# Kernel tuning notes

Hardware: AMD Instinct MI355X
Metric: run time of the kernel (lower is better)

Reference implementation:

```python
import jax, jax.numpy as jnp
import numpy as np
from jax import lax


def _conv(x, w, b):
    # x: [N,C,H,W], w: [O,I,kh,kw], valid conv, stride 1
    y = lax.conv_general_dilated(x, w, (1, 1), 'VALID',
                                 dimension_numbers=('NCHW', 'OIHW', 'NCHW'))
    return y + b[None, :, None, None]


def _maxpool2(x):
    return lax.reduce_window(x, -jnp.inf, lax.max, (1, 1, 2, 2), (1, 1, 2, 2), 'VALID')


def _affine_grid(theta, H, W):
    # torch F.affine_grid, align_corners=False: pixel-center normalized coords
    dt = theta.dtype
    xs = (2.0 * jnp.arange(W, dtype=dt) + 1.0) / W - 1.0  # [W]
    ys = (2.0 * jnp.arange(H, dtype=dt) + 1.0) / H - 1.0  # [H]
    gx = (theta[:, 0, 0][:, None, None] * xs[None, None, :]
          + theta[:, 0, 1][:, None, None] * ys[None, :, None]
          + theta[:, 0, 2][:, None, None])  # [N,H,W]
    gy = (theta[:, 1, 0][:, None, None] * xs[None, None, :]
          + theta[:, 1, 1][:, None, None] * ys[None, :, None]
          + theta[:, 1, 2][:, None, None])  # [N,H,W]
    return gx, gy


def _grid_sample(img, gx, gy):
    # torch F.grid_sample, bilinear, zeros padding, align_corners=False
    N, C, H, W = img.shape
    ix = ((gx + 1.0) * W - 1.0) * 0.5
    iy = ((gy + 1.0) * H - 1.0) * 0.5
    x0 = jnp.floor(ix)
    y0 = jnp.floor(iy)
    x1 = x0 + 1.0
    y1 = y0 + 1.0
    wx1 = ix - x0
    wx0 = 1.0 - wx1
    wy1 = iy - y0
    wy0 = 1.0 - wy1
    flat = img.reshape(N, C, H * W)

    def tap(xf, yf):
        xi = xf.astype(jnp.int32)
        yi = yf.astype(jnp.int32)
        inb = (xi >= 0) & (xi < W) & (yi >= 0) & (yi < H)
        idx = jnp.clip(yi, 0, H - 1) * W + jnp.clip(xi, 0, W - 1)  # [N,H,W]
        v = jnp.take_along_axis(flat, idx.reshape(N, 1, H * W), axis=2)
        return v.reshape(N, C, H, W) * inb.astype(img.dtype)[:, None]

    out = (tap(x0, y0) * (wx0 * wy0)[:, None]
           + tap(x1, y0) * (wx1 * wy0)[:, None]
           + tap(x0, y1) * (wx0 * wy1)[:, None]
           + tap(x1, y1) * (wx1 * wy1)[:, None])
    return out


def setup_inputs() -> dict:
    key = jax.random.key(0)
    ks = jax.random.split(key, 8)
    b, n, d, c = 64, 256, 28, 3
    x = jax.random.normal(ks[0], (b, n, d, d, c), dtype=jnp.float32)
    conv1_w = jax.random.normal(ks[1], (8, 3, 7, 7), dtype=jnp.float32) * 0.08
    conv1_b = jnp.zeros((8,), dtype=jnp.float32)
    conv2_w = jax.random.normal(ks[2], (10, 8, 5, 5), dtype=jnp.float32) * 0.07
    conv2_b = jnp.zeros((10,), dtype=jnp.float32)
    fc1_w = jax.random.normal(ks[3], (32, 90), dtype=jnp.float32) * 0.1
    fc1_b = jnp.zeros((32,), dtype=jnp.float32)
    # fc2 initialized near identity transform (as in the torch module),
    # with a small perturbation so theta depends on the input
    fc2_w = jax.random.normal(ks[4], (6, 32), dtype=jnp.float32) * 0.01
    fc2_b = jnp.array([1.0, 0.0, 0.0, 0.0, 1.0, 0.0], dtype=jnp.float32)
    return {"x": x, "conv1_w": conv1_w, "conv1_b": conv1_b,
            "conv2_w": conv2_w, "conv2_b": conv2_b,
            "fc1_w": fc1_w, "fc1_b": fc1_b,
            "fc2_w": fc2_w, "fc2_b": fc2_b}


def reference(x, conv1_w, conv1_b, conv2_w, conv2_b, fc1_w, fc1_b, fc2_w, fc2_b):
    b, n, d, _, c = x.shape
    xi = x.reshape(-1, d, d, c).transpose(0, 3, 1, 2)  # [b*n, 3, 28, 28]
    # localization net: conv -> maxpool -> relu, twice
    h = jax.nn.relu(_maxpool2(_conv(xi, conv1_w, conv1_b)))   # [N,8,11,11]
    h = jax.nn.relu(_maxpool2(_conv(h, conv2_w, conv2_b)))    # [N,10,3,3]
    h = h.reshape(-1, 10 * 3 * 3)
    h = jax.nn.relu(h @ fc1_w.T + fc1_b)
    theta = (h @ fc2_w.T + fc2_b).reshape(-1, 2, 3)
    gx, gy = _affine_grid(theta, d, d)
    out = _grid_sample(xi, gx, gy)                            # [N,3,28,28]
    return out.transpose(0, 2, 3, 1).reshape(b, n, d, d, c)
```

## Files before the change

### kernel.cpp

```cpp
#include <hip/hip_runtime.h>


typedef _Float16 half2_t __attribute__((ext_vector_type(2)));

static __device__ inline half2_t h2(uint32_t u) {
    union { uint32_t u; half2_t h; } cv; cv.u = u; return cv.h;
}

#if __has_builtin(__builtin_amdgcn_fdot2)
#define FDOT2(a, b, c) __builtin_amdgcn_fdot2((a), (b), (c), false)
#else
#define FDOT2(a, b, c) ((float)(a)[0] * (float)(b)[0] + (float)(a)[1] * (float)(b)[1] + (c))
#endif

__launch_bounds__(256, 4)
__global__ void stn_loc_kernel(
    const float* __restrict__ x,
    const float* __restrict__ w1, const float* __restrict__ b1,
    const float* __restrict__ w2, const float* __restrict__ b2,
    const float* __restrict__ fc1w, const float* __restrict__ fc1b,
    const float* __restrict__ fc2w, const float* __restrict__ fc2b,
    float* __restrict__ theta_ws)
{
    __shared__ __align__(16) _Float16 s_imgh[3 * 28 * 40];
    __shared__ __align__(16) uint32_t s_w1p[8 * 21 * 4];
    __shared__ __align__(16) float s_h1[8 * 11 * 12];
    __shared__ float s_h2[90];
    __shared__ float s_fch[32];

    const int t = threadIdx.x;
    const int n = blockIdx.x;
    const float* img = x + (size_t)n * 2352;

    for (int idx = t; idx < 504; idx += 256) {
        const int cc = idx / 168;
        const int rem = idx - 168 * cc;
        const int hh = rem / 6;
        const int kk = rem - 6 * hh;
        ((uint32_t*)s_imgh)[(((cc * 28 + hh) * 40) + 28 + 2 * kk) >> 1] = 0u;
    }
    for (int p = t; p < 784; p += 256) {
        const int h = p / 28, w = p - 28 * h;
        const float v0 = img[3 * p + 0];
        const float v1 = img[3 * p + 1];
        const float v2 = img[3 * p + 2];
        s_imgh[(0 * 28 + h) * 40 + w] = (_Float16)v0;
        s_imgh[(1 * 28 + h) * 40 + w] = (_Float16)v1;
        s_imgh[(2 * 28 + h) * 40 + w] = (_Float16)v2;
    }
    for (int idx = t; idx < 672; idx += 256) {
        const int o = idx / 84;  const int rem = idx - 84 * o;
        const int c = rem / 28;  const int r2 = rem - 28 * c;
        const int kh = r2 >> 2;  const int p = r2 & 3;
        const int k0 = 2 * p;
        const float* wbase = &w1[((o * 3 + c) * 7 + kh) * 7];
        const float wa = wbase[k0];
        const float wb = (k0 + 1 < 7) ? wbase[k0 + 1] : 0.0f;
        union { half2_t h; uint32_t u; } cv;
        cv.h = (half2_t){(_Float16)wa, (_Float16)wb};
        s_w1p[idx] = cv.u;
    }
    __syncthreads();

    if (t < 176) {
        const int i = t >> 3, o = t & 7;
        float acc[22];
        const float bias = b1[o];
        #pragma unroll
        for (int j = 0; j < 22; ++j) acc[j] = bias;

        for (int c = 0; c < 3; ++c) {
            #pragma unroll
            for (int kh = 0; kh < 7; ++kh) {
                const uint32_t* rowu =
                    (const uint32_t*)&s_imgh[(c * 28 + i + kh) * 40];
                uint32_t E[16];
                {
                    const uint4 a = ((const uint4*)rowu)[0];
                    const uint4 b = ((const uint4*)rowu)[1];
                    const uint4 cq = ((const uint4*)rowu)[2];
                    const uint4 d = ((const uint4*)rowu)[3];
                    E[0] = a.x;  E[1] = a.y;  E[2] = a.z;  E[3] = a.w;
                    E[4] = b.x;  E[5] = b.y;  E[6] = b.z;  E[7] = b.w;
                    E[8] = cq.x; E[9] = cq.y; E[10] = cq.z; E[11] = cq.w;
                    E[12] = d.x; E[13] = d.y; E[14] = d.z; E[15] = d.w;
                }
                uint32_t O[14];
                #pragma unroll
                for (int k = 0; k < 14; ++k)
                    O[k] = (E[k] >> 16) | (E[k + 1] << 16);

                const uint4 wq = *(const uint4*)&s_w1p[(o * 21 + c * 7 + kh) * 4];
                const half2_t wp0 = h2(wq.x), wp1 = h2(wq.y);
                const half2_t wp2 = h2(wq.z), wp3 = h2(wq.w);

                #pragma unroll
                for (int j = 0; j < 22; j += 2) {
                    const int b0 = j >> 1;
                    acc[j]     = FDOT2(h2(E[b0]),     wp0, acc[j]);
                    acc[j]     = FDOT2(h2(E[b0 + 1]), wp1, acc[j]);
                    acc[j]     = FDOT2(h2(E[b0 + 2]), wp2, acc[j]);
                    acc[j]     = FDOT2(h2(E[b0 + 3]), wp3, acc[j]);
                    acc[j + 1] = FDOT2(h2(O[b0]),     wp0, acc[j + 1]);
                    acc[j + 1] = FDOT2(h2(O[b0 + 1]), wp1, acc[j + 1]);
                    acc[j + 1] = FDOT2(h2(O[b0 + 2]), wp2, acc[j + 1]);
                    acc[j + 1] = FDOT2(h2(O[b0 + 3]), wp3, acc[j + 1]);
                }
            }
        }
        float hm[11];
        #pragma unroll
        for (int j = 0; j < 11; ++j) hm[j] = fmaxf(acc[2 * j], acc[2 * j + 1]);
        #pragma unroll
        for (int j = 0; j < 11; ++j) {
            float v = __shfl_xor(hm[j], 8);
            hm[j] = fmaxf(hm[j], v);
        }
        if ((i & 1) == 0) {
            float* row = &s_h1[(o * 11 + (i >> 1)) * 12];
            #pragma unroll
            for (int j = 0; j < 11; ++j) row[j] = fmaxf(hm[j], 0.0f);
        }
    }
    __syncthreads();

    if (t < 60) {
        const int o = t / 6, i = t - 6 * (t / 6);
        float acc2[6];
        const float bias = b2[o];
        #pragma unroll
        for (int j = 0; j < 6; ++j) acc2[j] = bias;
        for (int c = 0; c < 8; ++c) {
            #pragma unroll
            for (int kh = 0; kh < 5; ++kh) {
                const float* hrow = &s_h1[(c * 11 + i + kh) * 12];
                float im2[12];
                #pragma unroll
                for (int qq = 0; qq < 3; ++qq) {
                    float4 v = ((const float4*)hrow)[qq];
                    im2[4 * qq + 0] = v.x; im2[4 * qq + 1] = v.y;
                    im2[4 * qq + 2] = v.z; im2[4 * qq + 3] = v.w;
                }
                const float* wr = &w2[(o * 8 + c) * 25 + kh * 5];
                float wv[5];
                #pragma unroll
                for (int qq = 0; qq < 5; ++qq) wv[qq] = wr[qq];
                #pragma unroll
                for (int kw = 0; kw < 5; ++kw) {
                    #pragma unroll
                    for (int j = 0; j < 6; ++j)
                        acc2[j] += im2[j + kw] * wv[kw];
                }
            }
        }
        float hp[3];
        #pragma unroll
        for (int qq = 0; qq < 3; ++qq) hp[qq] = fmaxf(acc2[2 * qq], acc2[2 * qq + 1]);
        #pragma unroll
        for (int qq = 0; qq < 3; ++qq) {
            float v = __shfl_xor(hp[qq], 1);
            hp[qq] = fmaxf(hp[qq], v);
        }
        if ((i & 1) == 0) {
            #pragma unroll
            for (int qq = 0; qq < 3; ++qq)
                s_h2[o * 9 + (i >> 1) * 3 + qq] = fmaxf(hp[qq], 0.0f);
        }
    }
    __syncthreads();

    {
        const int of = t >> 3, l = t & 7;
        float acc = 0.0f;
        const float* wr = &fc1w[of * 90];
        #pragma unroll
        for (int m = 0; m < 12; ++m) {
            int j = l + 8 * m;
            if (j < 90) acc += s_h2[j] * wr[j];
        }
        acc += __shfl_xor(acc, 1);
        acc += __shfl_xor(acc, 2);
        acc += __shfl_xor(acc, 4);
        if (l == 0) s_fch[of] = fmaxf(acc + fc1b[of], 0.0f);
    }
    __syncthreads();

    if (t < 48) {
        const int of = t >> 3, l = t & 7;
        float acc = 0.0f;
        const float* wr = &fc2w[of * 32];
        #pragma unroll
        for (int m = 0; m < 4; ++m) {
            int j = l + 8 * m;
            acc += s_fch[j] * wr[j];
        }
        acc += __shfl_xor(acc, 1);
        acc += __shfl_xor(acc, 2);
        acc += __shfl_xor(acc, 4);
        if (l == 0) theta_ws[(size_t)n * 6 + of] = acc + fc2b[of];
    }
}

__launch_bounds__(256)
__global__ void stn_sample_kernel(
    const float* __restrict__ x,
    const float* __restrict__ theta_ws,
    float* __restrict__ out)
{
    const int t = threadIdx.x;
    const int n = blockIdx.x;
    const float* tw = theta_ws + (size_t)n * 6;
    const float t00 = tw[0], t01 = tw[1], t02 = tw[2];
    const float t10 = tw[3], t11 = tw[4], t12 = tw[5];
    const float* img = x + (size_t)n * 2352;
    float* outp = out + (size_t)n * 2352;

    for (int p = t; p < 784; p += 256) {
        int h = p / 28, w = p - 28 * h;
        float xs = (2.0f * w + 1.0f) * (1.0f / 28.0f) - 1.0f;
        float ys = (2.0f * h + 1.0f) * (1.0f / 28.0f) - 1.0f;
        float gx = t00 * xs + t01 * ys + t02;
        float gy = t10 * xs + t11 * ys + t12;
        float ix = ((gx + 1.0f) * 28.0f - 1.0f) * 0.5f;
        float iy = ((gy + 1.0f) * 28.0f - 1.0f) * 0.5f;
        float x0f = floorf(ix), y0f = floorf(iy);
        float wx1 = ix - x0f, wx0 = 1.0f - wx1;
        float wy1 = iy - y0f, wy0 = 1.0f - wy1;
        int x0 = (int)x0f, y0 = (int)y0f;
        int x1 = x0 + 1, y1 = y0 + 1;
        float fx0 = (x0 >= 0 && x0 < 28) ? 1.0f : 0.0f;
        float fx1 = (x1 >= 0 && x1 < 28) ? 1.0f : 0.0f;
        float fy0 = (y0 >= 0 && y0 < 28) ? 1.0f : 0.0f;
        float fy1 = (y1 >= 0 && y1 < 28) ? 1.0f : 0.0f;
        float w00 = wx0 * wy0 * fx0 * fy0;
        float w10 = wx1 * wy0 * fx1 * fy0;
        float w01 = wx0 * wy1 * fx0 * fy1;
        float w11 = wx1 * wy1 * fx1 * fy1;
        int cx0 = min(max(x0, 0), 27), cx1 = min(max(x1, 0), 27);
        int cy0 = min(max(y0, 0), 27), cy1 = min(max(y1, 0), 27);
        const float* p00 = img + (cy0 * 28 + cx0) * 3;
        const float* p10 = img + (cy0 * 28 + cx1) * 3;
        const float* p01 = img + (cy1 * 28 + cx0) * 3;
        const float* p11 = img + (cy1 * 28 + cx1) * 3;
        float* o3 = outp + 3 * p;
        #pragma unroll
        for (int c = 0; c < 3; ++c) {
            o3[c] = p00[c] * w00 + p10[c] * w10 + p01[c] * w01 + p11[c] * w11;
        }
    }
}

extern "C" void kernel_launch(void* const* d_in, const int* in_sizes, int n_in,
                              void* d_out, int out_size, void* d_ws, size_t ws_size,
                              hipStream_t stream) {
    const float* x     = (const float*)d_in[0];
    const float* w1    = (const float*)d_in[1];
    const float* b1    = (const float*)d_in[2];
    const float* w2    = (const float*)d_in[3];
    const float* b2    = (const float*)d_in[4];
    const float* fc1w  = (const float*)d_in[5];
    const float* fc1b  = (const float*)d_in[6];
    const float* fc2w  = (const float*)d_in[7];
    const float* fc2b  = (const float*)d_in[8];
    float* outp  = (float*)d_out;
    float* theta = (float*)d_ws;

    const int n_img = 64 * 256;
    stn_loc_kernel<<<dim3(n_img), dim3(256), 0, stream>>>(
        x, w1, b1, w2, b2, fc1w, fc1b, fc2w, fc2b, theta);
    stn_sample_kernel<<<dim3(n_img), dim3(256), 0, stream>>>(x, theta, outp);
}
```

Before: 313.2 us.

## Pack conv2 and fc1 operands as fp16 pairs and use fdot2

```diff
diff --git a/kernel.cpp b/kernel.cpp
--- a/kernel.cpp
+++ b/kernel.cpp
@@ -5,6 +5,11 @@
 
 static __device__ inline half2_t h2(uint32_t u) {
     union { uint32_t u; half2_t h; } cv; cv.u = u; return cv.h;
+}
+static __device__ inline uint32_t packh2(float a, float b) {
+    union { half2_t h; uint32_t u; } cv;
+    cv.h = (half2_t){(_Float16)a, (_Float16)b};
+    return cv.u;
 }
 
 #if __has_builtin(__builtin_amdgcn_fdot2)
@@ -24,8 +29,10 @@
 {
     __shared__ __align__(16) _Float16 s_imgh[3 * 28 * 40];
     __shared__ __align__(16) uint32_t s_w1p[8 * 21 * 4];
-    __shared__ __align__(16) float s_h1[8 * 11 * 12];
-    __shared__ float s_h2[90];
+    __shared__ __align__(16) uint32_t s_h1p[4 * 11 * 12];
+    __shared__ __align__(16) uint32_t s_w2p[4 * 5 * 10 * 8];
+    __shared__ __align__(16) uint32_t s_fc1wp[32 * 49];
+    __shared__ __align__(16) uint32_t s_h2p[64];
     __shared__ float s_fch[32];
 
     const int t = threadIdx.x;
@@ -56,18 +63,38 @@
         const float* wbase = &w1[((o * 3 + c) * 7 + kh) * 7];
         const float wa = wbase[k0];
         const float wb = (k0 + 1 < 7) ? wbase[k0 + 1] : 0.0f;
-        union { half2_t h; uint32_t u; } cv;
-        cv.h = (half2_t){(_Float16)wa, (_Float16)wb};
-        s_w1p[idx] = cv.u;
-    }
+        s_w1p[idx] = packh2(wa, wb);
+    }
+    for (int k = t; k < 1600; k += 256) {
+        const int kw = k & 7;
+        const int r = k >> 3;
+        const int o = r % 10;
+        const int ck = r / 10;
+        const int kh = ck % 5;
+        const int c2 = ck / 5;
+        uint32_t v = 0;
+        if (kw < 5) {
+            const float wa = w2[((o * 8 + 2 * c2) * 5 + kh) * 5 + kw];
+            const float wb = w2[((o * 8 + 2 * c2 + 1) * 5 + kh) * 5 + kw];
+            v = packh2(wa, wb);
+        }
+        s_w2p[k] = v;
+    }
+    for (int k = t; k < 1568; k += 256) {
+        const int of = k / 49;
+        const int j = k - 49 * of;
+        uint32_t v = 0;
+        if (j < 45) v = packh2(fc1w[of * 90 + 2 * j], fc1w[of * 90 + 2 * j + 1]);
+        s_fc1wp[k] = v;
+    }
+    if (t < 64) s_h2p[t] = 0;
     __syncthreads();
 
     if (t < 176) {
         const int i = t >> 3, o = t & 7;
         float acc[22];
-        const float bias = b1[o];
-        #pragma unroll
-        for (int j = 0; j < 22; ++j) acc[j] = bias;
+        #pragma unroll
+        for (int j = 0; j < 22; ++j) acc[j] = 0.0f;
 
         for (int c = 0; c < 3; ++c) {
             #pragma unroll
@@ -108,6 +135,7 @@
                 }
             }
         }
+        const float bias = b1[o];
         float hm[11];
         #pragma unroll
         for (int j = 0; j < 11; ++j) hm[j] = fmaxf(acc[2 * j], acc[2 * j + 1]);
@@ -117,9 +145,11 @@
             hm[j] = fmaxf(hm[j], v);
         }
         if ((i & 1) == 0) {
-            float* row = &s_h1[(o * 11 + (i >> 1)) * 12];
+            const int c2 = o >> 1, hf = o & 1, u = i >> 1;
+            _Float16* dst = ((_Float16*)s_h1p) + ((c2 * 11 + u) * 12) * 2 + hf;
             #pragma unroll
-            for (int j = 0; j < 11; ++j) row[j] = fmaxf(hm[j], 0.0f);
+            for (int m = 0; m < 11; ++m)
+                dst[2 * m] = (_Float16)fmaxf(hm[m] + bias, 0.0f);
         }
     }
     __syncthreads();
@@ -127,44 +157,53 @@
     if (t < 60) {
         const int o = t / 6, i = t - 6 * (t / 6);
         float acc2[6];
-        const float bias = b2[o];
-        #pragma unroll
-        for (int j = 0; j < 6; ++j) acc2[j] = bias;
-        for (int c = 0; c < 8; ++c) {
+        #pragma unroll
+        for (int j = 0; j < 6; ++j) acc2[j] = 0.0f;
+        #pragma unroll
+        for (int c2 = 0; c2 < 4; ++c2) {
             #pragma unroll
             for (int kh = 0; kh < 5; ++kh) {
-                const float* hrow = &s_h1[(c * 11 + i + kh) * 12];
-                float im2[12];
+                const uint32_t* row = &s_h1p[(c2 * 11 + i + kh) * 12];
+                uint32_t E[12];
+                {
+                    const uint4 a = ((const uint4*)row)[0];
+                    const uint4 b = ((const uint4*)row)[1];
+                    const uint4 cq = ((const uint4*)row)[2];
+                    E[0] = a.x;  E[1] = a.y;  E[2] = a.z;  E[3] = a.w;
+                    E[4] = b.x;  E[5] = b.y;  E[6] = b.z;  E[7] = b.w;
+                    E[8] = cq.x; E[9] = cq.y; E[10] = cq.z; E[11] = cq.w;
+                }
+                const uint32_t* wb = &s_w2p[((c2 * 5 + kh) * 10 + o) * 8];
+                const uint4 wq = *(const uint4*)wb;
+                const uint32_t w4 = wb[4];
+                const half2_t wp0 = h2(wq.x), wp1 = h2(wq.y), wp2 = h2(wq.z),
+                              wp3 = h2(wq.w), wp4 = h2(w4);
                 #pragma unroll
-                for (int qq = 0; qq < 3; ++qq) {
-                    float4 v = ((const float4*)hrow)[qq];
-                    im2[4 * qq + 0] = v.x; im2[4 * qq + 1] = v.y;
-                    im2[4 * qq + 2] = v.z; im2[4 * qq + 3] = v.w;
-                }
-                const float* wr = &w2[(o * 8 + c) * 25 + kh * 5];
-                float wv[5];
-                #pragma unroll
-                for (int qq = 0; qq < 5; ++qq) wv[qq] = wr[qq];
-                #pragma unroll
-                for (int kw = 0; kw < 5; ++kw) {
-                    #pragma unroll
-                    for (int j = 0; j < 6; ++j)
-                        acc2[j] += im2[j + kw] * wv[kw];
+                for (int j = 0; j < 6; ++j) {
+                    float a = acc2[j];
+                    a = FDOT2(h2(E[j]),     wp0, a);
+                    a = FDOT2(h2(E[j + 1]), wp1, a);
+                    a = FDOT2(h2(E[j + 2]), wp2, a);
+                    a = FDOT2(h2(E[j + 3]), wp3, a);
+                    a = FDOT2(h2(E[j + 4]), wp4, a);
+                    acc2[j] = a;
                 }
             }
         }
+        const float bias = b2[o];
         float hp[3];
         #pragma unroll
-        for (int qq = 0; qq < 3; ++qq) hp[qq] = fmaxf(acc2[2 * qq], acc2[2 * qq + 1]);
-        #pragma unroll
-        for (int qq = 0; qq < 3; ++qq) {
-            float v = __shfl_xor(hp[qq], 1);
-            hp[qq] = fmaxf(hp[qq], v);
+        for (int q = 0; q < 3; ++q) hp[q] = fmaxf(acc2[2 * q], acc2[2 * q + 1]);
+        #pragma unroll
+        for (int q = 0; q < 3; ++q) {
+            float v = __shfl_xor(hp[q], 1);
+            hp[q] = fmaxf(hp[q], v);
         }
         if ((i & 1) == 0) {
             #pragma unroll
-            for (int qq = 0; qq < 3; ++qq)
-                s_h2[o * 9 + (i >> 1) * 3 + qq] = fmaxf(hp[qq], 0.0f);
+            for (int q = 0; q < 3; ++q)
+                ((_Float16*)s_h2p)[o * 9 + (i >> 1) * 3 + q] =
+                    (_Float16)fmaxf(hp[q] + bias, 0.0f);
         }
     }
     __syncthreads();
@@ -172,11 +211,11 @@
     {
         const int of = t >> 3, l = t & 7;
         float acc = 0.0f;
-        const float* wr = &fc1w[of * 90];
-        #pragma unroll
-        for (int m = 0; m < 12; ++m) {
-            int j = l + 8 * m;
-            if (j < 90) acc += s_h2[j] * wr[j];
+        const uint32_t* wr = &s_fc1wp[of * 49];
+        #pragma unroll
+        for (int m = 0; m < 6; ++m) {
+            const int j = l + 8 * m;
+            acc = FDOT2(h2(s_h2p[j]), h2(wr[j]), acc);
         }
         acc += __shfl_xor(acc, 1);
         acc += __shfl_xor(acc, 2);
```

Result: slower. 349.1 us (+11.5%).

## Batch four images per block in localization kernel to raise thread utilization

Applied to the files above, without the earlier changes.

```diff
diff --git a/kernel.cpp b/kernel.cpp
--- a/kernel.cpp
+++ b/kernel.cpp
@@ -5,6 +5,11 @@
 
 static __device__ inline half2_t h2(uint32_t u) {
     union { uint32_t u; half2_t h; } cv; cv.u = u; return cv.h;
+}
+static __device__ inline uint32_t packh2(float a, float b) {
+    union { half2_t h; uint32_t u; } cv;
+    cv.h = (half2_t){(_Float16)a, (_Float16)b};
+    return cv.u;
 }
 
 #if __has_builtin(__builtin_amdgcn_fdot2)
@@ -22,31 +27,30 @@
     const float* __restrict__ fc2w, const float* __restrict__ fc2b,
     float* __restrict__ theta_ws)
 {
-    __shared__ __align__(16) _Float16 s_imgh[3 * 28 * 40];
+    __shared__ __align__(16) _Float16 s_imgh[4][3 * 28 * 40];
     __shared__ __align__(16) uint32_t s_w1p[8 * 21 * 4];
-    __shared__ __align__(16) float s_h1[8 * 11 * 12];
-    __shared__ float s_h2[90];
-    __shared__ float s_fch[32];
+    __shared__ __align__(16) float s_h1[4][8 * 11 * 12];
+    __shared__ float s_h2[4][90];
+    __shared__ float s_fch[4][32];
 
     const int t = threadIdx.x;
-    const int n = blockIdx.x;
-    const float* img = x + (size_t)n * 2352;
-
-    for (int idx = t; idx < 504; idx += 256) {
-        const int cc = idx / 168;
-        const int rem = idx - 168 * cc;
-        const int hh = rem / 6;
-        const int kk = rem - 6 * hh;
-        ((uint32_t*)s_imgh)[(((cc * 28 + hh) * 40) + 28 + 2 * kk) >> 1] = 0u;
-    }
-    for (int p = t; p < 784; p += 256) {
-        const int h = p / 28, w = p - 28 * h;
-        const float v0 = img[3 * p + 0];
-        const float v1 = img[3 * p + 1];
-        const float v2 = img[3 * p + 2];
-        s_imgh[(0 * 28 + h) * 40 + w] = (_Float16)v0;
-        s_imgh[(1 * 28 + h) * 40 + w] = (_Float16)v1;
-        s_imgh[(2 * 28 + h) * 40 + w] = (_Float16)v2;
+    const int nb = blockIdx.x;
+
+    for (int im = 0; im < 4; ++im) {
+        const float* img = x + ((size_t)(nb * 4 + im)) * 2352;
+        for (int p = t; p < 784; p += 256) {
+            const int h = p / 28, w = p - 28 * h;
+            s_imgh[im][(0 * 28 + h) * 40 + w] = (_Float16)img[3 * p + 0];
+            s_imgh[im][(1 * 28 + h) * 40 + w] = (_Float16)img[3 * p + 1];
+            s_imgh[im][(2 * 28 + h) * 40 + w] = (_Float16)img[3 * p + 2];
+        }
+        for (int idx = t; idx < 504; idx += 256) {
+            const int cc = idx / 168;
+            const int rem = idx - 168 * cc;
+            const int hh = rem / 6;
+            const int kk = rem - 6 * hh;
+            ((uint32_t*)s_imgh[im])[(((cc * 28 + hh) * 40) + 28 + 2 * kk) >> 1] = 0u;
+        }
     }
     for (int idx = t; idx < 672; idx += 256) {
         const int o = idx / 84;  const int rem = idx - 84 * o;
@@ -56,24 +60,23 @@
         const float* wbase = &w1[((o * 3 + c) * 7 + kh) * 7];
         const float wa = wbase[k0];
         const float wb = (k0 + 1 < 7) ? wbase[k0 + 1] : 0.0f;
-        union { half2_t h; uint32_t u; } cv;
-        cv.h = (half2_t){(_Float16)wa, (_Float16)wb};
-        s_w1p[idx] = cv.u;
-    }
-    __syncthreads();
-
-    if (t < 176) {
-        const int i = t >> 3, o = t & 7;
+        s_w1p[idx] = packh2(wa, wb);
+    }
+    __syncthreads();
+
+    for (int u = t; u < 704; u += 256) {
+        const int im = u / 176;
+        const int r  = u - 176 * im;
+        const int i = r >> 3, o = r & 7;
         float acc[22];
-        const float bias = b1[o];
-        #pragma unroll
-        for (int j = 0; j < 22; ++j) acc[j] = bias;
+        #pragma unroll
+        for (int j = 0; j < 22; ++j) acc[j] = 0.0f;
 
         for (int c = 0; c < 3; ++c) {
             #pragma unroll
             for (int kh = 0; kh < 7; ++kh) {
                 const uint32_t* rowu =
-                    (const uint32_t*)&s_imgh[(c * 28 + i + kh) * 40];
+                    (const uint32_t*)&s_imgh[im][(c * 28 + i + kh) * 40];
                 uint32_t E[16];
                 {
                     const uint4 a = ((const uint4*)rowu)[0];
@@ -108,6 +111,7 @@
                 }
             }
         }
+        const float bias = b1[o];
         float hm[11];
         #pragma unroll
         for (int j = 0; j < 11; ++j) hm[j] = fmaxf(acc[2 * j], acc[2 * j + 1]);
@@ -117,15 +121,17 @@
             hm[j] = fmaxf(hm[j], v);
         }
         if ((i & 1) == 0) {
-            float* row = &s_h1[(o * 11 + (i >> 1)) * 12];
-            #pragma unroll
-            for (int j = 0; j < 11; ++j) row[j] = fmaxf(hm[j], 0.0f);
-        }
-    }
-    __syncthreads();
-
-    if (t < 60) {
-        const int o = t / 6, i = t - 6 * (t / 6);
+            float* row = &s_h1[im][(o * 11 + (i >> 1)) * 12];
+            #pragma unroll
+            for (int j = 0; j < 11; ++j) row[j] = fmaxf(hm[j] + bias, 0.0f);
+        }
+    }
+    __syncthreads();
+
+    if (t < 240) {
+        const int im = t / 60;
+        const int r = t - 60 * im;
+        const int o = r / 6, i = r - 6 * (r / 6);
         float acc2[6];
         const float bias = b2[o];
         #pragma unroll
@@ -133,7 +139,7 @@
         for (int c = 0; c < 8; ++c) {
             #pragma unroll
             for (int kh = 0; kh < 5; ++kh) {
-                const float* hrow = &s_h1[(c * 11 + i + kh) * 12];
+                const float* hrow = &s_h1[im][(c * 11 + i + kh) * 12];
                 float im2[12];
                 #pragma unroll
                 for (int qq = 0; qq < 3; ++qq) {
@@ -164,40 +170,42 @@
         if ((i & 1) == 0) {
             #pragma unroll
             for (int qq = 0; qq < 3; ++qq)
-                s_h2[o * 9 + (i >> 1) * 3 + qq] = fmaxf(hp[qq], 0.0f);
+                s_h2[im][o * 9 + (i >> 1) * 3 + qq] = fmaxf(hp[qq], 0.0f);
         }
     }
     __syncthreads();
 
     {
-        const int of = t >> 3, l = t & 7;
+        const int im = t >> 6;
+        const int of = (t >> 1) & 31;
+        const int l = t & 1;
         float acc = 0.0f;
         const float* wr = &fc1w[of * 90];
         #pragma unroll
-        for (int m = 0; m < 12; ++m) {
-            int j = l + 8 * m;
-            if (j < 90) acc += s_h2[j] * wr[j];
+        for (int j = 0; j < 45; ++j) {
+            const int jj = l + 2 * j;
+            acc += s_h2[im][jj] * wr[jj];
+        }
+        acc += __shfl_xor(acc, 1);
+        if (l == 0) s_fch[im][of] = fmaxf(acc + fc1b[of], 0.0f);
+    }
+    __syncthreads();
+
+    if (t < 192) {
+        const int im = t / 48;
+        const int r = t - 48 * im;
+        const int of = r >> 3, l = r & 7;
+        float acc = 0.0f;
+        const float* wr = &fc2w[of * 32];
+        #pragma unroll
+        for (int m = 0; m < 4; ++m) {
+            const int j = l + 8 * m;
+            acc += s_fch[im][j] * wr[j];
         }
         acc += __shfl_xor(acc, 1);
         acc += __shfl_xor(acc, 2);
         acc += __shfl_xor(acc, 4);
-        if (l == 0) s_fch[of] = fmaxf(acc + fc1b[of], 0.0f);
-    }
-    __syncthreads();
-
-    if (t < 48) {
-        const int of = t >> 3, l = t & 7;
-        float acc = 0.0f;
-        const float* wr = &fc2w[of * 32];
-        #pragma unroll
-        for (int m = 0; m < 4; ++m) {
-            int j = l + 8 * m;
-            acc += s_fch[j] * wr[j];
-        }
-        acc += __shfl_xor(acc, 1);
-        acc += __shfl_xor(acc, 2);
-        acc += __shfl_xor(acc, 4);
-        if (l == 0) theta_ws[(size_t)n * 6 + of] = acc + fc2b[of];
+        if (l == 0) theta_ws[((size_t)(nb * 4 + im)) * 6 + of] = acc + fc2b[of];
     }
 }
 
@@ -266,7 +274,7 @@
     float* theta = (float*)d_ws;
 
     const int n_img = 64 * 256;
-    stn_loc_kernel<<<dim3(n_img), dim3(256), 0, stream>>>(
+    stn_loc_kernel<<<dim3(n_img / 4), dim3(256), 0, stream>>>(
         x, w1, b1, w2, b2, fc1w, fc1b, fc2w, fc2b, theta);
     stn_sample_kernel<<<dim3(n_img), dim3(256), 0, stream>>>(x, theta, outp);
 }
```

Result: no change. 312.3 us (-0.3%).
